# Kernel tuning notes

Hardware: AMD Instinct MI355X
Metric: run time of the kernel (lower is better)

Reference implementation:

```python
import jax, jax.numpy as jnp
import numpy as np

N = 100000      # nodes
E = 1600000     # edges (avg degree 16)
F_IN = 300      # input feature dim
H = 64          # hidden channels
OUT = 20        # output classes
L = 8           # num GCN2Conv layers
ALPHA = 0.1
THETA = 0.5


def setup_inputs() -> dict:
    key = jax.random.key(0)
    ks = jax.random.split(key, 6)
    x = jax.random.normal(ks[0], (N, F_IN), jnp.float32)
    edge_index = jax.random.randint(ks[1], (2, E), 0, N, dtype=jnp.int32)
    edge_weights = jax.random.uniform(ks[2], (E,), jnp.float32)
    W_in = jax.random.normal(ks[3], (F_IN, H), jnp.float32) / np.sqrt(F_IN)
    b_in = jnp.zeros((H,), jnp.float32)
    conv_w = jax.random.normal(ks[4], (L, H, H), jnp.float32) / np.sqrt(H)
    W_out = jax.random.normal(ks[5], (H, OUT), jnp.float32) / np.sqrt(H)
    b_out = jnp.zeros((OUT,), jnp.float32)
    return dict(x=x, edge_index=edge_index, edge_weights=edge_weights,
                W_in=W_in, b_in=b_in, conv_w=conv_w, W_out=W_out, b_out=b_out)


def _gcn_norm(edge_index, edge_weights, n, dtype):
    # add self-loops with weight 1, symmetric normalization (PyG gcn_norm)
    loop = jnp.arange(n, dtype=edge_index.dtype)
    row = jnp.concatenate([edge_index[0], loop])
    col = jnp.concatenate([edge_index[1], loop])
    w = jnp.concatenate([edge_weights, jnp.ones((n,), dtype)])
    deg = jax.ops.segment_sum(w, col, num_segments=n)
    dinv = jnp.where(deg > 0, jax.lax.rsqrt(deg), 0.0).astype(dtype)
    norm = dinv[row] * w * dinv[col]
    return row, col, norm


def reference(x, edge_index, edge_weights, W_in, b_in, conv_w, W_out, b_out):
    n = x.shape[0]
    row, col, norm = _gcn_norm(edge_index, edge_weights, n, x.dtype)
    # eval mode: dropout is identity
    h = jax.nn.relu(x @ W_in + b_in)   # start_with_lin (F_IN != H)
    x0 = h
    num_layers = conv_w.shape[0]
    for l in range(num_layers):
        beta = float(np.log(THETA / (l + 1) + 1.0))
        # A_hat @ h : gather sources, weight by norm, scatter-add to targets
        agg = jax.ops.segment_sum(norm[:, None] * h[row], col, num_segments=n)
        z = (1.0 - ALPHA) * agg + ALPHA * x0  # initial-residual mixing
        h = jax.nn.relu((1.0 - beta) * z + beta * (z @ conv_w[l]))
    return h @ W_out + b_out
```

## Files before the change

### kernel.cpp

```cpp
#include <hip/hip_runtime.h>
#include <hip/hip_fp16.h>
#include <math.h>


#define HID 64
#define FIN 300
#define NOUT 20
#define ALPHA 0.1f
#define DSCALE 262144.0f
#define CNT_SHIFT 25
#define DEG_MASK 0x1FFFFFFu
#define FBLK 1024

typedef _Float16 f16;
typedef f16 f16x8 __attribute__((ext_vector_type(8)));
typedef float f32x4 __attribute__((ext_vector_type(4)));

__device__ __forceinline__ float wdec(unsigned v) {
    union { unsigned short u; __half h; } c;
    c.u = (unsigned short)(v >> 17);
    return __half2float(c.h);
}

__device__ __forceinline__ void unpack8(const float4& v, float* f) {
    const __half2* p = reinterpret_cast<const __half2*>(&v);
#pragma unroll
    for (int i = 0; i < 4; ++i) {
        float2 t = __half22float2(p[i]);
        f[2 * i] = t.x;
        f[2 * i + 1] = t.y;
    }
}

__global__ __launch_bounds__(256) void accum_k(const int* __restrict__ row,
                                               const int* __restrict__ col,
                                               const float* __restrict__ ew,
                                               unsigned* __restrict__ packed,
                                               uint2* __restrict__ rec, int e, int n) {
    int xcd = blockIdx.x & 7;
    int lo = (int)(((long long)n * xcd) >> 3);
    int hi = (int)(((long long)n * (xcd + 1)) >> 3);
    int nblk = gridDim.x >> 3;
    int stride = nblk * 256;
    for (int i = (blockIdx.x >> 3) * 256 + threadIdx.x; i < e; i += stride) {
        int c = col[i];
        if (c < lo || c >= hi) continue;
        int r = row[i];
        float wv = ew[i];
        unsigned q = (unsigned)__float2uint_rn(wv * DSCALE);
        unsigned old = atomicAdd(&packed[c], (1u << CNT_SHIFT) | q);
        unsigned rank = (old >> CNT_SHIFT) & 0x7Fu;
        union { __half h; unsigned short u; } cv;
        cv.h = __float2half(wv);
        rec[i] = make_uint2((unsigned)c | (rank << 17),
                            (unsigned)r | ((unsigned)cv.u << 17));
    }
}

__global__ __launch_bounds__(1024) void unpackscan_k(const unsigned* __restrict__ packed,
                                                     float* __restrict__ dinv,
                                                     int* __restrict__ padcnt,
                                                     int* __restrict__ bsum, int n) {
    __shared__ int ws[16];
    int t = threadIdx.x, i = blockIdx.x * 1024 + t;
    int pad = 0;
    if (i < n) {
        unsigned v = packed[i];
        int cnt = (int)(v >> CNT_SHIFT);
        float d = 1.0f + (float)(v & DEG_MASK) * (1.0f / DSCALE);
        dinv[i] = rsqrtf(d);
        pad = (cnt + 3) & ~3;
        padcnt[i] = pad;
    }
    int s = pad;
#pragma unroll
    for (int d = 1; d < 64; d <<= 1) s += __shfl_xor(s, d);
    if ((t & 63) == 0) ws[t >> 6] = s;
    __syncthreads();
    if (t == 0) {
        int tot = 0;
#pragma unroll
        for (int k = 0; k < 16; ++k) tot += ws[k];
        bsum[blockIdx.x] = tot;
    }
}

__global__ void scan2_k(int* __restrict__ bsum, int nb, int* __restrict__ rp, int n) {
    int lane = threadIdx.x;
    int acc = 0;
    for (int base = 0; base < nb; base += 64) {
        int idx = base + lane;
        int orig = (idx < nb) ? bsum[idx] : 0;
        int v = orig;
#pragma unroll
        for (int d = 1; d < 64; d <<= 1) {
            int u = __shfl_up(v, d);
            if (lane >= d) v += u;
        }
        if (idx < nb) bsum[idx] = acc + v - orig;
        acc += __shfl(v, 63);
    }
    if (lane == 0) rp[n] = acc;
}

__global__ __launch_bounds__(1024) void scan3_k(const int* __restrict__ padcnt,
                                                const int* __restrict__ bsum,
                                                int* __restrict__ rp, int n) {
    __shared__ int ws[16];
    int t = threadIdx.x, i = blockIdx.x * 1024 + t;
    int lane = t & 63, w = t >> 6;
    int v = (i < n) ? padcnt[i] : 0;
    int sv = v;
#pragma unroll
    for (int d = 1; d < 64; d <<= 1) {
        int u = __shfl_up(sv, d);
        if (lane >= d) sv += u;
    }
    if (lane == 63) ws[w] = sv;
    __syncthreads();
    if (w == 0) {
        int x = (lane < 16) ? ws[lane] : 0;
#pragma unroll
        for (int d = 1; d < 16; d <<= 1) {
            int u = __shfl_up(x, d);
            if (lane >= d) x += u;
        }
        if (lane < 16) ws[lane] = x;
    }
    __syncthreads();
    int woff = (w > 0) ? ws[w - 1] : 0;
    if (i < n) rp[i] = bsum[blockIdx.x] + woff + sv - v;
}

__global__ void wt_k(const float* __restrict__ Win, f16* __restrict__ Wt) {
    int i = blockIdx.x * blockDim.x + threadIdx.x;
    if (i < 64 * 320) {
        int c = i / 320, k = i - c * 320;
        Wt[i] = (k < FIN) ? (f16)Win[k * 64 + c] : (f16)0.0f;
    }
}

__global__ __launch_bounds__(256) void fgi_k(const uint2* __restrict__ rec,
                                             const float* __restrict__ dinv,
                                             const int* __restrict__ rp,
                                             unsigned* __restrict__ edges, int e,
                                             const float* __restrict__ x,
                                             const f16* __restrict__ Wt,
                                             const float* __restrict__ bin,
                                             __half* __restrict__ x0h, int n) {
    __shared__ f16 As[64 * 72];
    int t = threadIdx.x;
    if (blockIdx.x < FBLK) {
        int xcd = blockIdx.x & 7;
        int lo = (int)(((long long)n * xcd) >> 3);
        int hi = (int)(((long long)n * (xcd + 1)) >> 3);
        int stride = (FBLK >> 3) * 256;
        for (int i = (blockIdx.x >> 3) * 256 + t; i < e; i += stride) {
            uint2 rc = rec[i];
            int c = (int)(rc.x & 0x1FFFFu);
            if (c < lo || c >= hi) continue;
            int r = (int)(rc.y & 0x1FFFFu);
            union { unsigned short u; __half h; } ev;
            ev.u = (unsigned short)(rc.y >> 17);
            float nw = (1.0f - ALPHA) * dinv[r] * __half2float(ev.h) * dinv[c];
            union { __half h; unsigned short u; } cv;
            cv.h = __float2half(nw);
            int rank = (int)((rc.x >> 17) & 0x7Fu);
            edges[rp[c] + rank] = ((unsigned)cv.u << 17) | (unsigned)r;
        }
        return;
    }
    int lane = t & 63, wv = t >> 6;
    int node0 = (blockIdx.x - FBLK) * 64;
    int lr = lane & 15, kg = lane >> 4;
    int fi = t & 15, rowbase = t >> 4;
    f32x4 acc0 = {0, 0, 0, 0}, acc1 = {0, 0, 0, 0}, acc2 = {0, 0, 0, 0}, acc3 = {0, 0, 0, 0};
    float4 xr[4];
    auto loadchunk = [&](int c) {
#pragma unroll
        for (int it = 0; it < 4; ++it) {
            int row = rowbase + it * 16;
            int rr = node0 + row;
            rr = (rr < n) ? rr : (n - 1);
            int kbase = c * 64 + fi * 4;
            xr[it] = make_float4(0.f, 0.f, 0.f, 0.f);
            if (kbase < FIN)
                xr[it] = *reinterpret_cast<const float4*>(x + (size_t)rr * FIN + kbase);
        }
    };
    loadchunk(0);
    for (int c = 0; c < 5; ++c) {
        __syncthreads();
#pragma unroll
        for (int it = 0; it < 4; ++it) {
            int row = rowbase + it * 16;
            union { float2 f2; f16 h[4]; } u;
            u.h[0] = (f16)xr[it].x; u.h[1] = (f16)xr[it].y;
            u.h[2] = (f16)xr[it].z; u.h[3] = (f16)xr[it].w;
            *reinterpret_cast<float2*>(As + row * 72 + fi * 4) = u.f2;
        }
        __syncthreads();
        if (c < 4) loadchunk(c + 1);
#pragma unroll
        for (int ks = 0; ks < 2; ++ks) {
            f16x8 a = *(const f16x8*)(As + (wv * 16 + lr) * 72 + ks * 32 + kg * 8);
            const f16* wb = Wt + c * 64 + ks * 32 + kg * 8;
            f16x8 b0 = *(const f16x8*)(wb + (0 * 16 + lr) * 320);
            f16x8 b1 = *(const f16x8*)(wb + (1 * 16 + lr) * 320);
            f16x8 b2 = *(const f16x8*)(wb + (2 * 16 + lr) * 320);
            f16x8 b3 = *(const f16x8*)(wb + (3 * 16 + lr) * 320);
            acc0 = __builtin_amdgcn_mfma_f32_16x16x32_f16(a, b0, acc0, 0, 0, 0);
            acc1 = __builtin_amdgcn_mfma_f32_16x16x32_f16(a, b1, acc1, 0, 0, 0);
            acc2 = __builtin_amdgcn_mfma_f32_16x16x32_f16(a, b2, acc2, 0, 0, 0);
            acc3 = __builtin_amdgcn_mfma_f32_16x16x32_f16(a, b3, acc3, 0, 0, 0);
        }
    }
    float bi0 = bin[0 * 16 + lr], bi1 = bin[1 * 16 + lr];
    float bi2 = bin[2 * 16 + lr], bi3 = bin[3 * 16 + lr];
    f16 ov[4][4];
#pragma unroll
    for (int r = 0; r < 4; ++r) {
        ov[0][r] = (f16)fmaxf(acc0[r] + bi0, 0.f);
        ov[1][r] = (f16)fmaxf(acc1[r] + bi1, 0.f);
        ov[2][r] = (f16)fmaxf(acc2[r] + bi2, 0.f);
        ov[3][r] = (f16)fmaxf(acc3[r] + bi3, 0.f);
    }
    __syncthreads();
#pragma unroll
    for (int cg = 0; cg < 4; ++cg)
#pragma unroll
        for (int r = 0; r < 4; ++r)
            As[(wv * 16 + kg * 4 + r) * 72 + cg * 16 + lr] = ov[cg][r];
    __syncthreads();
#pragma unroll
    for (int it = 0; it < 2; ++it) {
        int idx = t + it * 256;
        int row = idx >> 3, ch = idx & 7;
        int node = node0 + row;
        if (node < n)
            ((float4*)(x0h + (size_t)node * 64))[ch] =
                *reinterpret_cast<const float4*>(As + row * 72 + ch * 8);
    }
}

__global__ __launch_bounds__(256) void layer_k(const int* __restrict__ rp,
                                               const unsigned* __restrict__ edges,
                                               const float* __restrict__ dinv,
                                               const __half* __restrict__ x0h,
                                               const __half* __restrict__ hin,
                                               __half* __restrict__ hout,
                                               const float* __restrict__ Wl,
                                               float beta, int n,
                                               const float* __restrict__ Wout,
                                               const float* __restrict__ bout,
                                               float* __restrict__ out) {
    __shared__ f16 As[64 * 72];
    __shared__ f16 Bs[64 * 72];
    int t = threadIdx.x, lane = t & 63, wv = t >> 6;
    int node0 = blockIdx.x * 64;
    for (int i = t; i < 4096; i += 256) {
        int k = i >> 6, c = i & 63;
        Bs[c * 72 + k] = (f16)Wl[i];
    }
    int g = lane >> 3, c8 = lane & 7;
#pragma unroll
    for (int pass = 0; pass < 2; ++pass) {
        int row = pass * 32 + wv * 8 + g;
        int node = node0 + row;
        int nd = (node < n) ? node : (n - 1);
        int j = rp[nd], end = (node < n) ? rp[nd + 1] : j;
        float a0[8], a1[8], a2[8], a3[8];
#pragma unroll
        for (int i = 0; i < 8; ++i) { a0[i] = 0.f; a1[i] = 0.f; a2[i] = 0.f; a3[i] = 0.f; }
        while (__any(j < end)) {
            if (j < end) {
                uint4 e4 = *reinterpret_cast<const uint4*>(edges + j);
                float w0 = wdec(e4.x), w1 = wdec(e4.y), w2 = wdec(e4.z), w3 = wdec(e4.w);
                float4 r0 = ((const float4*)(hin + (size_t)(e4.x & 0x1FFFF) * 64))[c8];
                float4 r1 = ((const float4*)(hin + (size_t)(e4.y & 0x1FFFF) * 64))[c8];
                float4 r2 = ((const float4*)(hin + (size_t)(e4.z & 0x1FFFF) * 64))[c8];
                float4 r3 = ((const float4*)(hin + (size_t)(e4.w & 0x1FFFF) * 64))[c8];
                float f0[8], f1[8], f2[8], f3[8];
                unpack8(r0, f0);
                unpack8(r1, f1);
                unpack8(r2, f2);
                unpack8(r3, f3);
#pragma unroll
                for (int i = 0; i < 8; ++i) {
                    a0[i] = fmaf(w0, f0[i], a0[i]);
                    a1[i] = fmaf(w1, f1[i], a1[i]);
                    a2[i] = fmaf(w2, f2[i], a2[i]);
                    a3[i] = fmaf(w3, f3[i], a3[i]);
                }
            }
            j += 4;
        }
        float di = dinv[nd];
        float c1 = (1.0f - ALPHA) * di * di;
        float4 hs4 = ((const float4*)(hin + (size_t)nd * 64))[c8];
        float4 xs4 = ((const float4*)(x0h + (size_t)nd * 64))[c8];
        float hf[8], xf[8];
        unpack8(hs4, hf);
        unpack8(xs4, xf);
        f16x8 zv8;
#pragma unroll
        for (int i = 0; i < 8; ++i)
            zv8[i] = (f16)fmaf(ALPHA, xf[i],
                               fmaf(c1, hf[i], (a0[i] + a1[i]) + (a2[i] + a3[i])));
        *(f16x8*)(As + row * 72 + c8 * 8) = zv8;
    }
    __syncthreads();
    int lr = lane & 15, kg = lane >> 4;
    f32x4 acc0 = {0, 0, 0, 0}, acc1 = {0, 0, 0, 0}, acc2 = {0, 0, 0, 0}, acc3 = {0, 0, 0, 0};
    f16x8 af0 = *(const f16x8*)(As + (wv * 16 + lr) * 72 + kg * 8);
    f16x8 af1 = *(const f16x8*)(As + (wv * 16 + lr) * 72 + 32 + kg * 8);
    {
        f16x8 b0 = *(const f16x8*)(Bs + (0 * 16 + lr) * 72 + kg * 8);
        f16x8 b1 = *(const f16x8*)(Bs + (0 * 16 + lr) * 72 + 32 + kg * 8);
        acc0 = __builtin_amdgcn_mfma_f32_16x16x32_f16(af0, b0, acc0, 0, 0, 0);
        acc0 = __builtin_amdgcn_mfma_f32_16x16x32_f16(af1, b1, acc0, 0, 0, 0);
    }
    {
        f16x8 b0 = *(const f16x8*)(Bs + (1 * 16 + lr) * 72 + kg * 8);
        f16x8 b1 = *(const f16x8*)(Bs + (1 * 16 + lr) * 72 + 32 + kg * 8);
        acc1 = __builtin_amdgcn_mfma_f32_16x16x32_f16(af0, b0, acc1, 0, 0, 0);
        acc1 = __builtin_amdgcn_mfma_f32_16x16x32_f16(af1, b1, acc1, 0, 0, 0);
    }
    {
        f16x8 b0 = *(const f16x8*)(Bs + (2 * 16 + lr) * 72 + kg * 8);
        f16x8 b1 = *(const f16x8*)(Bs + (2 * 16 + lr) * 72 + 32 + kg * 8);
        acc2 = __builtin_amdgcn_mfma_f32_16x16x32_f16(af0, b0, acc2, 0, 0, 0);
        acc2 = __builtin_amdgcn_mfma_f32_16x16x32_f16(af1, b1, acc2, 0, 0, 0);
    }
    {
        f16x8 b0 = *(const f16x8*)(Bs + (3 * 16 + lr) * 72 + kg * 8);
        f16x8 b1 = *(const f16x8*)(Bs + (3 * 16 + lr) * 72 + 32 + kg * 8);
        acc3 = __builtin_amdgcn_mfma_f32_16x16x32_f16(af0, b0, acc3, 0, 0, 0);
        acc3 = __builtin_amdgcn_mfma_f32_16x16x32_f16(af1, b1, acc3, 0, 0, 0);
    }
    float omb = 1.0f - beta;
    f16 ov[4][4];
#pragma unroll
    for (int cg = 0; cg < 4; ++cg) {
        f32x4 acc = (cg == 0) ? acc0 : (cg == 1) ? acc1 : (cg == 2) ? acc2 : acc3;
        int col = cg * 16 + lr;
#pragma unroll
        for (int r = 0; r < 4; ++r) {
            float zv = (float)As[(wv * 16 + kg * 4 + r) * 72 + col];
            ov[cg][r] = (f16)fmaxf(fmaf(beta, acc[r], omb * zv), 0.f);
        }
    }
    __syncthreads();
#pragma unroll
    for (int cg = 0; cg < 4; ++cg)
#pragma unroll
        for (int r = 0; r < 4; ++r)
            As[(wv * 16 + kg * 4 + r) * 72 + cg * 16 + lr] = ov[cg][r];
    __syncthreads();

    if (!Wout) {
#pragma unroll
        for (int it = 0; it < 2; ++it) {
            int idx = t + it * 256;
            int row = idx >> 3, ch = idx & 7;
            int node = node0 + row;
            if (node < n)
                ((float4*)(hout + (size_t)node * 64))[ch] =
                    *reinterpret_cast<const float4*>(As + row * 72 + ch * 8);
        }
    } else {
        for (int i = t; i < 32 * 64; i += 256) {
            int c = i >> 6, k = i & 63;
            Bs[c * 72 + k] = (c < NOUT) ? (f16)Wout[k * NOUT + c] : (f16)0.0f;
        }
        __syncthreads();
        f16x8 ha0 = *(const f16x8*)(As + (wv * 16 + lr) * 72 + kg * 8);
        f16x8 ha1 = *(const f16x8*)(As + (wv * 16 + lr) * 72 + 32 + kg * 8);
#pragma unroll
        for (int ct = 0; ct < 2; ++ct) {
            f32x4 oacc = {0, 0, 0, 0};
            f16x8 b0 = *(const f16x8*)(Bs + (ct * 16 + lr) * 72 + kg * 8);
            f16x8 b1 = *(const f16x8*)(Bs + (ct * 16 + lr) * 72 + 32 + kg * 8);
            oacc = __builtin_amdgcn_mfma_f32_16x16x32_f16(ha0, b0, oacc, 0, 0, 0);
            oacc = __builtin_amdgcn_mfma_f32_16x16x32_f16(ha1, b1, oacc, 0, 0, 0);
            int col = ct * 16 + lr;
            if (col < NOUT) {
                float bo = bout[col];
#pragma unroll
                for (int r = 0; r < 4; ++r) {
                    int nd2 = node0 + wv * 16 + kg * 4 + r;
                    if (nd2 < n) out[(size_t)nd2 * NOUT + col] = oacc[r] + bo;
                }
            }
        }
    }
}

extern "C" void kernel_launch(void* const* d_in, const int* in_sizes, int n_in,
                              void* d_out, int out_size, void* d_ws, size_t ws_size,
                              hipStream_t stream) {
    const float* x    = (const float*)d_in[0];
    const int*   ei   = (const int*)d_in[1];
    const float* ew   = (const float*)d_in[2];
    const float* Win  = (const float*)d_in[3];
    const float* bin  = (const float*)d_in[4];
    const float* cw   = (const float*)d_in[5];
    const float* Wout = (const float*)d_in[6];
    const float* bout = (const float*)d_in[7];

    const int n = in_sizes[0] / FIN;
    const int e = in_sizes[2];
    const int L = in_sizes[5] / (HID * HID);
    const int* row = ei;
    const int* col = ei + e;
    const int epadmax = e + 3 * n + 64;

    size_t off = 0;
    auto alloc = [&](size_t bytes) -> char* {
        char* q = (char*)d_ws + off;
        off = (off + bytes + 255) & ~(size_t)255;
        return q;
    };
    __half* x0h  = (__half*)alloc((size_t)n * HID * 2);
    __half* hA   = (__half*)alloc((size_t)n * HID * 2);
    __half* hB   = (__half*)alloc((size_t)n * HID * 2);
    unsigned* edges = (unsigned*)alloc((size_t)epadmax * 4);
    uint2* rec   = (uint2*)alloc((size_t)e * 8);
    unsigned* packed = (unsigned*)alloc((size_t)n * 4);
    float* dinv  = (float*)alloc((size_t)n * 4);
    int*   padcnt= (int*)alloc((size_t)n * 4);
    int*   rp    = (int*)alloc((size_t)(n + 1) * 4);
    int*   bsum  = (int*)alloc(1024 * 4);
    f16*   Wt    = (f16*)alloc((size_t)64 * 320 * 2);

    const int nb = (n + 1023) / 1024;
    const int ntile = (n + 63) / 64;

    hipMemsetAsync(packed, 0, (size_t)n * 4, stream);
    hipMemsetAsync(edges, 0, (size_t)epadmax * 4, stream);
    wt_k<<<(64 * 320 + 255) / 256, 256, 0, stream>>>(Win, Wt);
    accum_k<<<1024, 256, 0, stream>>>(row, col, ew, packed, rec, e, n);
    unpackscan_k<<<nb, 1024, 0, stream>>>(packed, dinv, padcnt, bsum, n);
    scan2_k<<<1, 64, 0, stream>>>(bsum, nb, rp, n);
    scan3_k<<<nb, 1024, 0, stream>>>(padcnt, bsum, rp, n);

    fgi_k<<<FBLK + ntile, 256, 0, stream>>>(rec, dinv, rp, edges, e,
                                            x, Wt, bin, x0h, n);

    const __half* hin = x0h;
    __half* hout = hA;
    for (int l = 0; l < L; ++l) {
        float beta = (float)log(0.5 / (double)(l + 1) + 1.0);
        bool last = (l == L - 1);
        layer_k<<<ntile, 256, 0, stream>>>(rp, edges, dinv, x0h, hin, hout,
                                           cw + (size_t)l * HID * HID, beta, n,
                                           last ? Wout : nullptr,
                                           last ? bout : nullptr,
                                           last ? (float*)d_out : nullptr);
        hin = hout;
        hout = (hout == hA) ? hB : hA;
    }
}
```

Measured before the change: 490.0 us.

## Overlap degree accumulation with input GEMM and unroll gather loop by eight

The edge atomic-accumulation pass now runs in the same launch as the input-projection MFMA GEMM, and the CSR fill pass becomes a standalone kernel. The atomic pass no longer filters edges by XCD-partitioned column range, so it loses that locality in exchange for sharing the GPU with the compute-bound GEMM. The layer aggregation loop now issues two groups of four edge gathers before consuming them, raising memory-level parallelism at the cost of more registers.

```diff
diff --git a/kernel.cpp b/kernel.cpp
--- a/kernel.cpp
+++ b/kernel.cpp
@@ -10,7 +10,7 @@
 #define DSCALE 262144.0f
 #define CNT_SHIFT 25
 #define DEG_MASK 0x1FFFFFFu
-#define FBLK 1024
+#define ABLK 2048
 
 typedef _Float16 f16;
 typedef f16 f16x8 __attribute__((ext_vector_type(8)));
@@ -29,31 +29,6 @@
         float2 t = __half22float2(p[i]);
         f[2 * i] = t.x;
         f[2 * i + 1] = t.y;
-    }
-}
-
-__global__ __launch_bounds__(256) void accum_k(const int* __restrict__ row,
-                                               const int* __restrict__ col,
-                                               const float* __restrict__ ew,
-                                               unsigned* __restrict__ packed,
-                                               uint2* __restrict__ rec, int e, int n) {
-    int xcd = blockIdx.x & 7;
-    int lo = (int)(((long long)n * xcd) >> 3);
-    int hi = (int)(((long long)n * (xcd + 1)) >> 3);
-    int nblk = gridDim.x >> 3;
-    int stride = nblk * 256;
-    for (int i = (blockIdx.x >> 3) * 256 + threadIdx.x; i < e; i += stride) {
-        int c = col[i];
-        if (c < lo || c >= hi) continue;
-        int r = row[i];
-        float wv = ew[i];
-        unsigned q = (unsigned)__float2uint_rn(wv * DSCALE);
-        unsigned old = atomicAdd(&packed[c], (1u << CNT_SHIFT) | q);
-        unsigned rank = (old >> CNT_SHIFT) & 0x7Fu;
-        union { __half h; unsigned short u; } cv;
-        cv.h = __float2half(wv);
-        rec[i] = make_uint2((unsigned)c | (rank << 17),
-                            (unsigned)r | ((unsigned)cv.u << 17));
     }
 }
 
@@ -132,6 +107,31 @@
     if (i < n) rp[i] = bsum[blockIdx.x] + woff + sv - v;
 }
 
+__global__ __launch_bounds__(256) void fill_k(const uint2* __restrict__ rec,
+                                              const float* __restrict__ dinv,
+                                              const int* __restrict__ rp,
+                                              unsigned* __restrict__ edges,
+                                              int e, int n) {
+    int xcd = blockIdx.x & 7;
+    int lo = (int)(((long long)n * xcd) >> 3);
+    int hi = (int)(((long long)n * (xcd + 1)) >> 3);
+    int nblk = gridDim.x >> 3;
+    int stride = nblk * 256;
+    for (int i = (blockIdx.x >> 3) * 256 + threadIdx.x; i < e; i += stride) {
+        uint2 rc = rec[i];
+        int c = (int)(rc.x & 0x1FFFFu);
+        if (c < lo || c >= hi) continue;
+        int r = (int)(rc.y & 0x1FFFFu);
+        union { unsigned short u; __half h; } ev;
+        ev.u = (unsigned short)(rc.y >> 17);
+        float nw = (1.0f - ALPHA) * dinv[r] * __half2float(ev.h) * dinv[c];
+        union { __half h; unsigned short u; } cv;
+        cv.h = __float2half(nw);
+        int rank = (int)((rc.x >> 17) & 0x7Fu);
+        edges[rp[c] + rank] = ((unsigned)cv.u << 17) | (unsigned)r;
+    }
+}
+
 __global__ void wt_k(const float* __restrict__ Win, f16* __restrict__ Wt) {
     int i = blockIdx.x * blockDim.x + threadIdx.x;
     if (i < 64 * 320) {
@@ -140,38 +140,33 @@
     }
 }
 
-__global__ __launch_bounds__(256) void fgi_k(const uint2* __restrict__ rec,
-                                             const float* __restrict__ dinv,
-                                             const int* __restrict__ rp,
-                                             unsigned* __restrict__ edges, int e,
+__global__ __launch_bounds__(256) void agi_k(const int* __restrict__ row,
+                                             const int* __restrict__ col,
+                                             const float* __restrict__ ew,
+                                             unsigned* __restrict__ packed,
+                                             uint2* __restrict__ rec, int e,
                                              const float* __restrict__ x,
                                              const f16* __restrict__ Wt,
                                              const float* __restrict__ bin,
                                              __half* __restrict__ x0h, int n) {
     __shared__ f16 As[64 * 72];
     int t = threadIdx.x;
-    if (blockIdx.x < FBLK) {
-        int xcd = blockIdx.x & 7;
-        int lo = (int)(((long long)n * xcd) >> 3);
-        int hi = (int)(((long long)n * (xcd + 1)) >> 3);
-        int stride = (FBLK >> 3) * 256;
-        for (int i = (blockIdx.x >> 3) * 256 + t; i < e; i += stride) {
-            uint2 rc = rec[i];
-            int c = (int)(rc.x & 0x1FFFFu);
-            if (c < lo || c >= hi) continue;
-            int r = (int)(rc.y & 0x1FFFFu);
-            union { unsigned short u; __half h; } ev;
-            ev.u = (unsigned short)(rc.y >> 17);
-            float nw = (1.0f - ALPHA) * dinv[r] * __half2float(ev.h) * dinv[c];
+    if (blockIdx.x < ABLK) {
+        for (int i = blockIdx.x * 256 + t; i < e; i += ABLK * 256) {
+            int c = col[i], r = row[i];
+            float wv = ew[i];
+            unsigned q = (unsigned)__float2uint_rn(wv * DSCALE);
+            unsigned old = atomicAdd(&packed[c], (1u << CNT_SHIFT) | q);
+            unsigned rank = (old >> CNT_SHIFT) & 0x7Fu;
             union { __half h; unsigned short u; } cv;
-            cv.h = __float2half(nw);
-            int rank = (int)((rc.x >> 17) & 0x7Fu);
-            edges[rp[c] + rank] = ((unsigned)cv.u << 17) | (unsigned)r;
+            cv.h = __float2half(wv);
+            rec[i] = make_uint2((unsigned)c | (rank << 17),
+                                (unsigned)r | ((unsigned)cv.u << 17));
         }
         return;
     }
     int lane = t & 63, wv = t >> 6;
-    int node0 = (blockIdx.x - FBLK) * 64;
+    int node0 = (blockIdx.x - ABLK) * 64;
     int lr = lane & 15, kg = lane >> 4;
     int fi = t & 15, rowbase = t >> 4;
     f32x4 acc0 = {0, 0, 0, 0}, acc1 = {0, 0, 0, 0}, acc2 = {0, 0, 0, 0}, acc3 = {0, 0, 0, 0};
@@ -179,8 +174,8 @@
     auto loadchunk = [&](int c) {
 #pragma unroll
         for (int it = 0; it < 4; ++it) {
-            int row = rowbase + it * 16;
-            int rr = node0 + row;
+            int rw = rowbase + it * 16;
+            int rr = node0 + rw;
             rr = (rr < n) ? rr : (n - 1);
             int kbase = c * 64 + fi * 4;
             xr[it] = make_float4(0.f, 0.f, 0.f, 0.f);
@@ -193,11 +188,11 @@
         __syncthreads();
 #pragma unroll
         for (int it = 0; it < 4; ++it) {
-            int row = rowbase + it * 16;
+            int rw = rowbase + it * 16;
             union { float2 f2; f16 h[4]; } u;
             u.h[0] = (f16)xr[it].x; u.h[1] = (f16)xr[it].y;
             u.h[2] = (f16)xr[it].z; u.h[3] = (f16)xr[it].w;
-            *reinterpret_cast<float2*>(As + row * 72 + fi * 4) = u.f2;
+            *reinterpret_cast<float2*>(As + rw * 72 + fi * 4) = u.f2;
         }
         __syncthreads();
         if (c < 4) loadchunk(c + 1);
@@ -235,11 +230,11 @@
 #pragma unroll
     for (int it = 0; it < 2; ++it) {
         int idx = t + it * 256;
-        int row = idx >> 3, ch = idx & 7;
-        int node = node0 + row;
+        int rw = idx >> 3, ch = idx & 7;
+        int node = node0 + rw;
         if (node < n)
             ((float4*)(x0h + (size_t)node * 64))[ch] =
-                *reinterpret_cast<const float4*>(As + row * 72 + ch * 8);
+                *reinterpret_cast<const float4*>(As + rw * 72 + ch * 8);
     }
 }
 
@@ -273,18 +268,28 @@
 #pragma unroll
         for (int i = 0; i < 8; ++i) { a0[i] = 0.f; a1[i] = 0.f; a2[i] = 0.f; a3[i] = 0.f; }
         while (__any(j < end)) {
-            if (j < end) {
-                uint4 e4 = *reinterpret_cast<const uint4*>(edges + j);
-                float w0 = wdec(e4.x), w1 = wdec(e4.y), w2 = wdec(e4.z), w3 = wdec(e4.w);
-                float4 r0 = ((const float4*)(hin + (size_t)(e4.x & 0x1FFFF) * 64))[c8];
-                float4 r1 = ((const float4*)(hin + (size_t)(e4.y & 0x1FFFF) * 64))[c8];
-                float4 r2 = ((const float4*)(hin + (size_t)(e4.z & 0x1FFFF) * 64))[c8];
-                float4 r3 = ((const float4*)(hin + (size_t)(e4.w & 0x1FFFF) * 64))[c8];
+            bool va = j < end;
+            bool vb = (j + 4) < end;
+            uint4 ea, eb;
+            float4 ra0, ra1, ra2, ra3, rb0, rb1, rb2, rb3;
+            if (va) ea = *reinterpret_cast<const uint4*>(edges + j);
+            if (vb) eb = *reinterpret_cast<const uint4*>(edges + j + 4);
+            if (va) {
+                ra0 = ((const float4*)(hin + (size_t)(ea.x & 0x1FFFF) * 64))[c8];
+                ra1 = ((const float4*)(hin + (size_t)(ea.y & 0x1FFFF) * 64))[c8];
+                ra2 = ((const float4*)(hin + (size_t)(ea.z & 0x1FFFF) * 64))[c8];
+                ra3 = ((const float4*)(hin + (size_t)(ea.w & 0x1FFFF) * 64))[c8];
+            }
+            if (vb) {
+                rb0 = ((const float4*)(hin + (size_t)(eb.x & 0x1FFFF) * 64))[c8];
+                rb1 = ((const float4*)(hin + (size_t)(eb.y & 0x1FFFF) * 64))[c8];
+                rb2 = ((const float4*)(hin + (size_t)(eb.z & 0x1FFFF) * 64))[c8];
+                rb3 = ((const float4*)(hin + (size_t)(eb.w & 0x1FFFF) * 64))[c8];
+            }
+            if (va) {
+                float w0 = wdec(ea.x), w1 = wdec(ea.y), w2 = wdec(ea.z), w3 = wdec(ea.w);
                 float f0[8], f1[8], f2[8], f3[8];
-                unpack8(r0, f0);
-                unpack8(r1, f1);
-                unpack8(r2, f2);
-                unpack8(r3, f3);
+                unpack8(ra0, f0); unpack8(ra1, f1); unpack8(ra2, f2); unpack8(ra3, f3);
 #pragma unroll
                 for (int i = 0; i < 8; ++i) {
                     a0[i] = fmaf(w0, f0[i], a0[i]);
@@ -293,7 +298,19 @@
                     a3[i] = fmaf(w3, f3[i], a3[i]);
                 }
             }
-            j += 4;
+            if (vb) {
+                float w0 = wdec(eb.x), w1 = wdec(eb.y), w2 = wdec(eb.z), w3 = wdec(eb.w);
+                float f0[8], f1[8], f2[8], f3[8];
+                unpack8(rb0, f0); unpack8(rb1, f1); unpack8(rb2, f2); unpack8(rb3, f3);
+#pragma unroll
+                for (int i = 0; i < 8; ++i) {
+                    a0[i] = fmaf(w0, f0[i], a0[i]);
+                    a1[i] = fmaf(w1, f1[i], a1[i]);
+                    a2[i] = fmaf(w2, f2[i], a2[i]);
+                    a3[i] = fmaf(w3, f3[i], a3[i]);
+                }
+            }
+            j += 8;
         }
         float di = dinv[nd];
         float c1 = (1.0f - ALPHA) * di * di;
@@ -439,13 +456,13 @@
     hipMemsetAsync(packed, 0, (size_t)n * 4, stream);
     hipMemsetAsync(edges, 0, (size_t)epadmax * 4, stream);
     wt_k<<<(64 * 320 + 255) / 256, 256, 0, stream>>>(Win, Wt);
-    accum_k<<<1024, 256, 0, stream>>>(row, col, ew, packed, rec, e, n);
+
+    agi_k<<<ABLK + ntile, 256, 0, stream>>>(row, col, ew, packed, rec, e,
+                                            x, Wt, bin, x0h, n);
     unpackscan_k<<<nb, 1024, 0, stream>>>(packed, dinv, padcnt, bsum, n);
     scan2_k<<<1, 64, 0, stream>>>(bsum, nb, rp, n);
     scan3_k<<<nb, 1024, 0, stream>>>(padcnt, bsum, rp, n);
-
-    fgi_k<<<FBLK + ntile, 256, 0, stream>>>(rec, dinv, rp, edges, e,
-                                            x, Wt, bin, x0h, n);
+    fill_k<<<1024, 256, 0, stream>>>(rec, dinv, rp, edges, e, n);
 
     const __half* hin = x0h;
     __half* hout = hA;
```

Result: slower. 584.1 us (+19.2%).

## Zero only padding slots in scan and simplify edge accumulation grid

Applied to the files above, without the earlier changes.

Drops the full-size memset of the padded edge array and instead has the scan kernel zero only each node's padding slots, past its real edge count. It also replaces the XCD-partitioned, grid-strided accumulation kernel with a plain one-thread-per-edge launch. The partitioned version had every block read all columns and skip most of them. The trade-off is that atomics on a node are no longer kept local to one XCD's L2, so they may contend more across dies. The rest of the change renames the 'row' locals to 'rw'.

```diff
diff --git a/kernel.cpp b/kernel.cpp
--- a/kernel.cpp
+++ b/kernel.cpp
@@ -32,20 +32,13 @@
     }
 }
 
-__global__ __launch_bounds__(256) void accum_k(const int* __restrict__ row,
-                                               const int* __restrict__ col,
-                                               const float* __restrict__ ew,
-                                               unsigned* __restrict__ packed,
-                                               uint2* __restrict__ rec, int e, int n) {
-    int xcd = blockIdx.x & 7;
-    int lo = (int)(((long long)n * xcd) >> 3);
-    int hi = (int)(((long long)n * (xcd + 1)) >> 3);
-    int nblk = gridDim.x >> 3;
-    int stride = nblk * 256;
-    for (int i = (blockIdx.x >> 3) * 256 + threadIdx.x; i < e; i += stride) {
-        int c = col[i];
-        if (c < lo || c >= hi) continue;
-        int r = row[i];
+__global__ void accum_k(const int* __restrict__ row, const int* __restrict__ col,
+                        const float* __restrict__ ew,
+                        unsigned* __restrict__ packed,
+                        uint2* __restrict__ rec, int e) {
+    int i = blockIdx.x * blockDim.x + threadIdx.x;
+    if (i < e) {
+        int c = col[i], r = row[i];
         float wv = ew[i];
         unsigned q = (unsigned)__float2uint_rn(wv * DSCALE);
         unsigned old = atomicAdd(&packed[c], (1u << CNT_SHIFT) | q);
@@ -104,8 +97,10 @@
 }
 
 __global__ __launch_bounds__(1024) void scan3_k(const int* __restrict__ padcnt,
+                                                const unsigned* __restrict__ packed,
                                                 const int* __restrict__ bsum,
-                                                int* __restrict__ rp, int n) {
+                                                int* __restrict__ rp,
+                                                unsigned* __restrict__ edges, int n) {
     __shared__ int ws[16];
     int t = threadIdx.x, i = blockIdx.x * 1024 + t;
     int lane = t & 63, w = t >> 6;
@@ -129,7 +124,12 @@
     }
     __syncthreads();
     int woff = (w > 0) ? ws[w - 1] : 0;
-    if (i < n) rp[i] = bsum[blockIdx.x] + woff + sv - v;
+    if (i < n) {
+        int base = bsum[blockIdx.x] + woff + sv - v;
+        rp[i] = base;
+        int cnt = (int)(packed[i] >> CNT_SHIFT);
+        for (int k = cnt; k < v; ++k) edges[base + k] = 0u;
+    }
 }
 
 __global__ void wt_k(const float* __restrict__ Win, f16* __restrict__ Wt) {
@@ -179,8 +179,8 @@
     auto loadchunk = [&](int c) {
 #pragma unroll
         for (int it = 0; it < 4; ++it) {
-            int row = rowbase + it * 16;
-            int rr = node0 + row;
+            int rw = rowbase + it * 16;
+            int rr = node0 + rw;
             rr = (rr < n) ? rr : (n - 1);
             int kbase = c * 64 + fi * 4;
             xr[it] = make_float4(0.f, 0.f, 0.f, 0.f);
@@ -193,11 +193,11 @@
         __syncthreads();
 #pragma unroll
         for (int it = 0; it < 4; ++it) {
-            int row = rowbase + it * 16;
+            int rw = rowbase + it * 16;
             union { float2 f2; f16 h[4]; } u;
             u.h[0] = (f16)xr[it].x; u.h[1] = (f16)xr[it].y;
             u.h[2] = (f16)xr[it].z; u.h[3] = (f16)xr[it].w;
-            *reinterpret_cast<float2*>(As + row * 72 + fi * 4) = u.f2;
+            *reinterpret_cast<float2*>(As + rw * 72 + fi * 4) = u.f2;
         }
         __syncthreads();
         if (c < 4) loadchunk(c + 1);
@@ -235,11 +235,11 @@
 #pragma unroll
     for (int it = 0; it < 2; ++it) {
         int idx = t + it * 256;
-        int row = idx >> 3, ch = idx & 7;
-        int node = node0 + row;
+        int rw = idx >> 3, ch = idx & 7;
+        int node = node0 + rw;
         if (node < n)
             ((float4*)(x0h + (size_t)node * 64))[ch] =
-                *reinterpret_cast<const float4*>(As + row * 72 + ch * 8);
+                *reinterpret_cast<const float4*>(As + rw * 72 + ch * 8);
     }
 }
 
@@ -362,11 +362,11 @@
 #pragma unroll
         for (int it = 0; it < 2; ++it) {
             int idx = t + it * 256;
-            int row = idx >> 3, ch = idx & 7;
-            int node = node0 + row;
+            int rw = idx >> 3, ch = idx & 7;
+            int node = node0 + rw;
             if (node < n)
                 ((float4*)(hout + (size_t)node * 64))[ch] =
-                    *reinterpret_cast<const float4*>(As + row * 72 + ch * 8);
+                    *reinterpret_cast<const float4*>(As + rw * 72 + ch * 8);
         }
     } else {
         for (int i = t; i < 32 * 64; i += 256) {
@@ -437,12 +437,11 @@
     const int ntile = (n + 63) / 64;
 
     hipMemsetAsync(packed, 0, (size_t)n * 4, stream);
-    hipMemsetAsync(edges, 0, (size_t)epadmax * 4, stream);
     wt_k<<<(64 * 320 + 255) / 256, 256, 0, stream>>>(Win, Wt);
-    accum_k<<<1024, 256, 0, stream>>>(row, col, ew, packed, rec, e, n);
+    accum_k<<<(e + 255) / 256, 256, 0, stream>>>(row, col, ew, packed, rec, e);
     unpackscan_k<<<nb, 1024, 0, stream>>>(packed, dinv, padcnt, bsum, n);
     scan2_k<<<1, 64, 0, stream>>>(bsum, nb, rp, n);
-    scan3_k<<<nb, 1024, 0, stream>>>(padcnt, bsum, rp, n);
+    scan3_k<<<nb, 1024, 0, stream>>>(padcnt, packed, bsum, rp, edges, n);
 
     fgi_k<<<FBLK + ntile, 256, 0, stream>>>(rec, dinv, rp, edges, e,
                                             x, Wt, bin, x0h, n);
```

Result: no change. 481.5 us (-1.7%).
